# Performance work log

Hardware: AMD Instinct MI355X
Metric: run time of the kernel (lower is better)

Reference implementation:

```python
import jax, jax.numpy as jnp
import numpy as np

B, S, M, E, H = 4, 2048, 1024, 8, 4096
CAP = 2 * (B * S) // E  # GShard top-2 capacity = 2*s/e = 2048


def setup_inputs() -> dict:
    key = jax.random.key(0)
    k = jax.random.split(key, 6)
    sc = 0.02
    return {
        "x": jax.random.normal(k[0], (B, S, M), jnp.float32),
        "wg": jax.random.normal(k[1], (M, E), jnp.float32) * sc,
        "w1": jax.random.normal(k[2], (E, M, H), jnp.float32) * sc,
        "b1": jnp.zeros((E, H), jnp.float32),
        "w2": jax.random.normal(k[3], (E, H, M), jnp.float32) * sc,
        "b2": jnp.zeros((E, M), jnp.float32),
    }


def top2gating(logits, capacity):
    # Faithful GShard/fairscale top2gating: logits [s, e]
    s, e = logits.shape
    gates = jax.nn.softmax(logits, axis=-1)
    idx1 = jnp.argmax(gates, axis=1)
    mask1 = jax.nn.one_hot(idx1, e, dtype=jnp.float32)
    logits2 = jnp.where(mask1 > 0, -jnp.inf, logits)
    idx2 = jnp.argmax(logits2, axis=1)
    mask2 = jax.nn.one_hot(idx2, e, dtype=jnp.float32)
    # positions within each expert's buffer
    loc1 = jnp.cumsum(mask1, axis=0) - 1.0
    loc2 = jnp.cumsum(mask2, axis=0) - 1.0 + jnp.sum(mask1, axis=0, keepdims=True)
    # load-balancing aux loss (computed before capacity drop, per fairscale)
    me = jnp.mean(gates, axis=0)
    ce = jnp.mean(mask1, axis=0)
    l_aux = jnp.mean(me * ce) * (e * e)
    # drop tokens over capacity
    mask1 = mask1 * (loc1 < capacity)
    mask2 = mask2 * (loc2 < capacity)
    loc1_s = jnp.sum(loc1 * mask1, axis=1).astype(jnp.int32)
    loc2_s = jnp.sum(loc2 * mask2, axis=1).astype(jnp.int32)
    gates1 = jnp.sum(gates * mask1, axis=1)
    gates2 = jnp.sum(gates * mask2, axis=1)
    denom = jnp.maximum(gates1 + gates2, 1e-9)
    gates1 = gates1 / denom
    gates2 = gates2 / denom
    # dense [s, e, c] combine weights (as in the original einsum formulation)
    oh1 = jax.nn.one_hot(loc1_s, capacity, dtype=jnp.float32)
    oh2 = jax.nn.one_hot(loc2_s, capacity, dtype=jnp.float32)
    combine = (gates1[:, None] * mask1)[:, :, None] * oh1[:, None, :] \
            + (gates2[:, None] * mask2)[:, :, None] * oh2[:, None, :]
    dispatch = combine > 0
    return l_aux, combine, dispatch


def reference(x, wg, w1, b1, w2, b2):
    d_model = x.shape[2]
    xf = x.reshape(-1, d_model)                      # [s, m]
    logits = xf @ wg                                 # [s, e]
    l_aux, combine, dispatch = top2gating(logits, CAP)
    # dispatch: dense one-hot scatter, as in torch.einsum('sec,sm->ecm')
    disp = jnp.einsum('sec,sm->ecm', dispatch.astype(xf.dtype), xf)
    # per-expert FFN (Linear -> ReLU -> Linear), vectorized over experts
    h = jax.nn.relu(jnp.einsum('ecm,emh->ech', disp, w1) + b1[:, None, :])
    eo = jnp.einsum('ech,ehm->ecm', h, w2) + b2[:, None, :]
    # combine: torch.einsum('sec,ecm->sm')
    out = jnp.einsum('sec,ecm->sm', combine, eo)
    return out.reshape(x.shape), l_aux
```

## Files before the change

kernel.cpp:

```cpp
#include <hip/hip_runtime.h>
#include <stdint.h>

typedef unsigned short u16;
typedef __attribute__((ext_vector_type(8))) short bf16x8;
typedef __attribute__((ext_vector_type(4))) float f32x4;

#define TOKENS 8192
#define DM 1024
#define NE 8
#define DH 4096
#define CAP 2048

__device__ __forceinline__ u16 f2bf(float f) {
  unsigned int u = __float_as_uint(f);
  u = u + 0x7FFFu + ((u >> 16) & 1u);
  return (u16)(u >> 16);
}

__device__ __forceinline__ void gll16(const void* g, void* l) {
  __builtin_amdgcn_global_load_lds(
      (const __attribute__((address_space(1))) unsigned int*)g,
      (__attribute__((address_space(3))) unsigned int*)l, 16, 0, 0);
}

__global__ __launch_bounds__(256) void gating_kernel(
    const float* __restrict__ x, const float* __restrict__ wg,
    int* __restrict__ idx1, int* __restrict__ idx2,
    float* __restrict__ g1r, float* __restrict__ g2r, float* __restrict__ me) {
  __shared__ float gsh[4][8];
  int lane = threadIdx.x & 63;
  int w = threadIdx.x >> 6;
  int t = blockIdx.x * 4 + w;
  const float* xr = x + (size_t)t * DM;
  double acc[8];
#pragma unroll
  for (int e = 0; e < 8; ++e) acc[e] = 0.0;
#pragma unroll
  for (int it = 0; it < 4; ++it) {
    float4 xv = ((const float4*)xr)[it * 64 + lane];
    int base = (it * 64 + lane) * 4;
    const float* wr = wg + (size_t)base * 8;
    float xs[4] = {xv.x, xv.y, xv.z, xv.w};
#pragma unroll
    for (int j = 0; j < 4; ++j)
#pragma unroll
      for (int e = 0; e < 8; ++e) acc[e] += (double)xs[j] * (double)wr[j * 8 + e];
  }
#pragma unroll
  for (int off = 32; off > 0; off >>= 1)
#pragma unroll
    for (int e = 0; e < 8; ++e) acc[e] += __shfl_down(acc[e], off);
  if (lane == 0) {
    float l[8];
#pragma unroll
    for (int e = 0; e < 8; ++e) l[e] = (float)acc[e];
    int i1 = 0;
    float v1 = l[0];
#pragma unroll
    for (int e = 1; e < 8; ++e)
      if (l[e] > v1) { v1 = l[e]; i1 = e; }
    int i2 = -1;
    float v2 = -3.4e38f;
#pragma unroll
    for (int e = 0; e < 8; ++e)
      if (e != i1 && l[e] > v2) { v2 = l[e]; i2 = e; }
    float s = 0.f;
    float p[8];
#pragma unroll
    for (int e = 0; e < 8; ++e) { p[e] = expf(l[e] - v1); s += p[e]; }
    float inv = 1.f / s;
    idx1[t] = i1;
    idx2[t] = i2;
    g1r[t] = inv;
    g2r[t] = expf(v2 - v1) * inv;
#pragma unroll
    for (int e = 0; e < 8; ++e) gsh[w][e] = p[e] * inv;
  }
  __syncthreads();
  if (threadIdx.x < 8) {
    int e = threadIdx.x;
    atomicAdd(&me[e], gsh[0][e] + gsh[1][e] + gsh[2][e] + gsh[3][e]);
  }
}

__global__ __launch_bounds__(1024) void scan_kernel(
    const int* __restrict__ idx1, const int* __restrict__ idx2,
    const float* __restrict__ g1r, const float* __restrict__ g2r,
    const float* __restrict__ me,
    int* __restrict__ slot1, int* __restrict__ slot2,
    float* __restrict__ g1n, float* __restrict__ g2n,
    int* __restrict__ slot2tok, float* __restrict__ laux) {
  __shared__ u16 c[16][1024];
  __shared__ u16 csum[16][32];
  __shared__ int tot[16];
  int tid = threadIdx.x;
  int i1[8], i2[8];
#pragma unroll
  for (int ctr = 0; ctr < 16; ++ctr) c[ctr][tid] = 0;
#pragma unroll
  for (int j = 0; j < 8; ++j) {
    int t = tid * 8 + j;
    i1[j] = idx1[t];
    i2[j] = idx2[t];
    c[i1[j]][tid]++;
    c[8 + i2[j]][tid]++;
  }
  __syncthreads();
  if (tid < 512) {
    int ctr = tid >> 5, ch = tid & 31;
    int s = 0;
#pragma unroll
    for (int i = 0; i < 32; ++i) s += c[ctr][ch * 32 + i];
    csum[ctr][ch] = (u16)s;
  }
  __syncthreads();
  if (tid < 16) {
    int run = 0;
#pragma unroll
    for (int ch = 0; ch < 32; ++ch) {
      int v = csum[tid][ch];
      csum[tid][ch] = (u16)run;
      run += v;
    }
    tot[tid] = run;
  }
  __syncthreads();
  if (tid < 512) {
    int ctr = tid >> 5, ch = tid & 31;
    int run = csum[ctr][ch];
#pragma unroll
    for (int i = 0; i < 32; ++i) {
      int v = c[ctr][ch * 32 + i];
      c[ctr][ch * 32 + i] = (u16)run;
      run += v;
    }
  }
  __syncthreads();
#pragma unroll
  for (int j = 0; j < 8; ++j) {
    int t = tid * 8 + j;
    int e1 = i1[j], e2 = i2[j];
    int L1 = c[e1][tid]++;
    int L2 = c[8 + e2][tid]++;
    L2 += tot[e2];
    bool kv1 = L1 < CAP, kv2 = L2 < CAP;
    float G1 = kv1 ? g1r[t] : 0.f;
    float G2 = kv2 ? g2r[t] : 0.f;
    float den = fmaxf(G1 + G2, 1e-9f);
    g1n[t] = G1 / den;
    g2n[t] = G2 / den;
    int s1 = kv1 ? (e1 * CAP + L1) : -1;
    int s2 = kv2 ? (e2 * CAP + L2) : -1;
    slot1[t] = s1;
    slot2[t] = s2;
    if (kv1) slot2tok[s1] = t;
    if (kv2) slot2tok[s2] = t;
  }
  if (tid == 0) {
    double a = 0.0;
    for (int e = 0; e < 8; ++e)
      a += ((double)me[e] / 8192.0) * ((double)tot[e] / 8192.0);
    laux[0] = (float)(a * 8.0);
  }
}

__global__ void transpose_kernel(const float* __restrict__ src, u16* __restrict__ dst,
                                 int R, int C) {
  __shared__ float tile[32][33];
  int tx = threadIdx.x, ty = threadIdx.y;
  int r0 = blockIdx.y * 32, c0 = blockIdx.x * 32;
  const float* s = src + (size_t)blockIdx.z * R * C;
  u16* d = dst + (size_t)blockIdx.z * R * C;
#pragma unroll
  for (int i = 0; i < 32; i += 8) tile[ty + i][tx] = s[(size_t)(r0 + ty + i) * C + c0 + tx];
  __syncthreads();
#pragma unroll
  for (int i = 0; i < 32; i += 8)
    d[(size_t)(c0 + ty + i) * R + r0 + tx] = f2bf(tile[tx][ty + i]);
}

__global__ void gather_kernel(const float* __restrict__ x, const int* __restrict__ slot2tok,
                              u16* __restrict__ xe) {
  int slot = blockIdx.y * CAP + blockIdx.x;
  int tok = slot2tok[slot];
  int tid = threadIdx.x;
  u16 o[8];
  if (tok >= 0) {
    const float4* xr = (const float4*)(x + (size_t)tok * DM);
    float4 a = xr[tid * 2], b = xr[tid * 2 + 1];
    o[0] = f2bf(a.x); o[1] = f2bf(a.y); o[2] = f2bf(a.z); o[3] = f2bf(a.w);
    o[4] = f2bf(b.x); o[5] = f2bf(b.y); o[6] = f2bf(b.z); o[7] = f2bf(b.w);
  } else {
#pragma unroll
    for (int j = 0; j < 8; ++j) o[j] = 0;
  }
  *(uint4*)(xe + (size_t)slot * DM + tid * 8) = *(const uint4*)o;
}

#define BAR()                              \
  {                                        \
    asm volatile("" ::: "memory");         \
    __builtin_amdgcn_s_barrier();          \
    asm volatile("" ::: "memory");         \
  }
#define VMCNT(n) asm volatile("s_waitcnt vmcnt(" #n ")" ::: "memory")
#define LGKM(n) asm volatile("s_waitcnt lgkmcnt(" #n ")" ::: "memory")

template <int RELU, int OUTBF16>
__global__ __launch_bounds__(512, 2) void gemm_kernel(
    const u16* __restrict__ A, const u16* __restrict__ Bt,
    const float* __restrict__ bias, void* __restrict__ Cv,
    int MO, int NO, int K) {
  __shared__ __align__(16) u16 As[2][256 * 64];
  __shared__ __align__(16) u16 Bs[2][256 * 64];
  const int tid = threadIdx.x;
  const int lane = tid & 63, wid = tid >> 6;
  const int wm = wid >> 2, wn = wid & 3;

  const int gx = gridDim.x, gy = gridDim.y;
  const int nwg = gx * gy * gridDim.z;
  const int L = (blockIdx.z * gy + blockIdx.y) * gx + blockIdx.x;
  const int cpx = nwg >> 3;
  const int Ls = (L & 7) * cpx + (L >> 3);
  const int bx = Ls % gx;
  const int tq = Ls / gx;
  const int by = tq % gy;
  const int eb = tq / gy;

  const size_t Ks2 = (size_t)K * 2;
  const char* Ag = (const char*)(A + (size_t)eb * MO * K + (size_t)by * 256 * K);
  const char* Bg = (const char*)(Bt + (size_t)eb * NO * K + (size_t)bx * 256 * K);
  const int rl = tid >> 3;
  const int sb = ((tid & 7) * 16) ^ ((rl & 7) << 4);
  Ag += (size_t)rl * Ks2 + sb;
  Bg += (size_t)rl * Ks2 + sb;
  char* AsB = ((char*)As) + tid * 16;
  char* BsB = ((char*)Bs) + tid * 16;
  const u16* AsE = &As[0][0];
  const u16* BsE = &Bs[0][0];
  const int fr = lane & 15, kg8 = (lane >> 4) * 8;
  const int swz = (fr & 7) << 3;

#define STAGE_A(BUF_, REG_, KT_) \
  gll16(Ag + (size_t)((REG_)*64) * Ks2 + (size_t)(KT_)*128, AsB + (BUF_)*32768 + (REG_)*8192)
#define STAGE_B(BUF_, REG_, KT_) \
  gll16(Bg + (size_t)((REG_)*64) * Ks2 + (size_t)(KT_)*128, BsB + (BUF_)*32768 + (REG_)*8192)
#define LDA(BUF_, M_, K_) \
  (*(const bf16x8*)&AsE[(BUF_)*16384 + (wm * 128 + (M_)*16 + fr) * 64 + (((K_)*32 + kg8) ^ swz)])
#define LDB(BUF_, N_, K_) \
  (*(const bf16x8*)&BsE[(BUF_)*16384 + (wn * 64 + (N_)*16 + fr) * 64 + (((K_)*32 + kg8) ^ swz)])
#define MFMA_Q(MB_, NB_)                                                            \
  _Pragma("unroll") for (int k = 0; k < 2; ++k)                                     \
  _Pragma("unroll") for (int m = 0; m < 4; ++m)                                     \
  _Pragma("unroll") for (int n = 0; n < 2; ++n)                                     \
      acc[(MB_) + m][(NB_) + n] = __builtin_amdgcn_mfma_f32_16x16x32_bf16(          \
          areg[m][k], breg[(NB_) + n][k], acc[(MB_) + m][(NB_) + n], 0, 0, 0)

#define RD_A03(C_)                                                \
  _Pragma("unroll") for (int m = 0; m < 4; ++m) {                 \
    areg[m][0] = LDA(C_, m, 0); areg[m][1] = LDA(C_, m, 1);       \
  }
#define RD_A47(C_)                                                \
  _Pragma("unroll") for (int m = 0; m < 4; ++m) {                 \
    areg[m][0] = LDA(C_, 4 + m, 0); areg[m][1] = LDA(C_, 4 + m, 1); \
  }
#define RD_B01(C_)                                                \
  _Pragma("unroll") for (int n = 0; n < 2; ++n) {                 \
    breg[n][0] = LDB(C_, n, 0); breg[n][1] = LDB(C_, n, 1);       \
  }
#define RD_B23(C_)                                                \
  _Pragma("unroll") for (int n = 2; n < 4; ++n) {                 \
    breg[n][0] = LDB(C_, n, 0); breg[n][1] = LDB(C_, n, 1);       \
  }
#define MM(MB_, NB_)                          \
  BAR();                                      \
  LGKM(0);                                    \
  __builtin_amdgcn_sched_barrier(0);          \
  __builtin_amdgcn_s_setprio(1);              \
  MFMA_Q(MB_, NB_);                           \
  __builtin_amdgcn_s_setprio(0);              \
  BAR();

  f32x4 acc[8][4];
#pragma unroll
  for (int i = 0; i < 8; ++i)
#pragma unroll
    for (int j = 0; j < 4; ++j) acc[i][j] = {0.f, 0.f, 0.f, 0.f};
  bf16x8 areg[4][2], breg[4][2];

  const int NT = K >> 6;

  STAGE_A(0, 0, 0); STAGE_A(0, 1, 0); STAGE_A(0, 2, 0); STAGE_A(0, 3, 0);
  STAGE_B(0, 0, 0); STAGE_B(0, 1, 0); STAGE_B(0, 2, 0); STAGE_B(0, 3, 0);
  STAGE_A(1, 0, 1); STAGE_A(1, 2, 1);
  STAGE_B(1, 0, 1); STAGE_B(1, 1, 1);
  STAGE_B(1, 2, 1); STAGE_B(1, 3, 1);
  VMCNT(6);
  BAR();

  for (int t = 0; t < NT; t += 2) {
    const int t2 = (t + 2 < NT) ? t + 2 : NT - 2;
    const int t3 = (t + 3 < NT) ? t + 3 : NT - 1;
    RD_A03(0); RD_B01(0);
    STAGE_A(1, 1, t + 1); STAGE_A(1, 3, t + 1);
    LGKM(8);
    MM(0, 0);
    RD_B23(0);
    STAGE_A(0, 0, t2); STAGE_A(0, 2, t2);
    MM(0, 2);
    RD_A47(0);
    STAGE_B(0, 0, t2); STAGE_B(0, 1, t2);
    MM(4, 0);
    STAGE_B(0, 2, t2); STAGE_B(0, 3, t2);
    VMCNT(6);
    MM(4, 2);
    RD_A03(1); RD_B01(1);
    STAGE_A(0, 1, t2); STAGE_A(0, 3, t2);
    LGKM(8);
    MM(0, 0);
    RD_B23(1);
    STAGE_A(1, 0, t3); STAGE_A(1, 2, t3);
    MM(0, 2);
    RD_A47(1);
    STAGE_B(1, 0, t3); STAGE_B(1, 1, t3);
    MM(4, 0);
    STAGE_B(1, 2, t3); STAGE_B(1, 3, t3);
    VMCNT(6);
    MM(4, 2);
  }

  const int row0 = by * 256 + wm * 128 + (kg8 >> 3) * 4;
  const int col0 = bx * 256 + wn * 64 + fr;
  const float* be = bias + (size_t)eb * NO;
  size_t cbase = (size_t)eb * MO * NO;
#pragma unroll
  for (int m = 0; m < 8; ++m) {
#pragma unroll
    for (int n = 0; n < 4; ++n) {
      int col = col0 + n * 16;
      float bv = be[col];
#pragma unroll
      for (int r = 0; r < 4; ++r) {
        int row = row0 + m * 16 + r;
        float v = acc[m][n][r] + bv;
        if (RELU) v = fmaxf(v, 0.f);
        if (OUTBF16)
          ((u16*)Cv)[cbase + (size_t)row * NO + col] = f2bf(v);
        else
          ((float*)Cv)[cbase + (size_t)row * NO + col] = v;
      }
    }
  }
#undef MM
#undef RD_A03
#undef RD_A47
#undef RD_B01
#undef RD_B23
#undef STAGE_A
#undef STAGE_B
#undef LDA
#undef LDB
#undef MFMA_Q
}

__global__ void combine_kernel(const float* __restrict__ eo,
                               const float* __restrict__ g1n, const float* __restrict__ g2n,
                               const int* __restrict__ slot1, const int* __restrict__ slot2,
                               float* __restrict__ out) {
  int t = blockIdx.x, tid = threadIdx.x;
  float g1 = g1n[t], g2 = g2n[t];
  int s1 = slot1[t], s2 = slot2[t];
  float4 o = make_float4(0.f, 0.f, 0.f, 0.f);
  if (s1 >= 0) {
    float4 a = ((const float4*)(eo + (size_t)s1 * DM))[tid];
    o.x = g1 * a.x; o.y = g1 * a.y; o.z = g1 * a.z; o.w = g1 * a.w;
  }
  if (s2 >= 0) {
    float4 b = ((const float4*)(eo + (size_t)s2 * DM))[tid];
    o.x += g2 * b.x; o.y += g2 * b.y; o.z += g2 * b.z; o.w += g2 * b.w;
  }
  ((float4*)(out + (size_t)t * DM))[tid] = o;
}

extern "C" void kernel_launch(void* const* d_in, const int* in_sizes, int n_in,
                              void* d_out, int out_size, void* d_ws, size_t ws_size,
                              hipStream_t stream) {
  const float* x = (const float*)d_in[0];
  const float* wg = (const float*)d_in[1];
  const float* w1 = (const float*)d_in[2];
  const float* b1 = (const float*)d_in[3];
  const float* w2 = (const float*)d_in[4];
  const float* b2 = (const float*)d_in[5];
  float* out = (float*)d_out;

  const size_t SZ_WT1 = (size_t)NE * DH * DM * 2;
  const size_t SZ_WT2 = (size_t)NE * DM * DH * 2;
  const size_t SZ_XE = (size_t)NE * CAP * DM * 2;
  const size_t SZ_H = (size_t)NE * CAP * DH * 2;
  const size_t SZ_TOK = (size_t)TOKENS * 4;

  char* p = (char*)d_ws;
  u16* wt1 = (u16*)p;
  float* eo = (float*)p;            p += SZ_WT1;
  u16* wt2 = (u16*)p;               p += SZ_WT2;
  u16* xe = (u16*)p;                p += SZ_XE;
  u16* h = (u16*)p;                 p += SZ_H;
  int* idx1 = (int*)p;              p += SZ_TOK;
  int* idx2 = (int*)p;              p += SZ_TOK;
  int* slot1 = (int*)p;             p += SZ_TOK;
  int* slot2 = (int*)p;             p += SZ_TOK;
  float* g1r = (float*)p;           p += SZ_TOK;
  float* g2r = (float*)p;           p += SZ_TOK;
  float* g1n = (float*)p;           p += SZ_TOK;
  float* g2n = (float*)p;           p += SZ_TOK;
  int* slot2tok = (int*)p;          p += (size_t)NE * CAP * 4;
  float* me = (float*)p;            p += 256;
  if ((size_t)(p - (char*)d_ws) > ws_size) return;

  hipMemsetAsync(me, 0, 32, stream);
  hipMemsetAsync(slot2tok, 0xFF, (size_t)NE * CAP * 4, stream);

  gating_kernel<<<TOKENS / 4, 256, 0, stream>>>(x, wg, idx1, idx2, g1r, g2r, me);
  scan_kernel<<<1, 1024, 0, stream>>>(idx1, idx2, g1r, g2r, me, slot1, slot2, g1n, g2n,
                                      slot2tok, out + (size_t)TOKENS * DM);
  transpose_kernel<<<dim3(DH / 32, DM / 32, NE), dim3(32, 8), 0, stream>>>(w1, wt1, DM, DH);
  transpose_kernel<<<dim3(DM / 32, DH / 32, NE), dim3(32, 8), 0, stream>>>(w2, wt2, DH, DM);
  gather_kernel<<<dim3(CAP, NE), 128, 0, stream>>>(x, slot2tok, xe);
  gemm_kernel<1, 1><<<dim3(DH / 256, CAP / 256, NE), 512, 0, stream>>>(xe, wt1, b1, (void*)h,
                                                                       CAP, DH, DM);
  gemm_kernel<0, 0><<<dim3(DM / 256, CAP / 256, NE), 512, 0, stream>>>(h, wt2, b2, (void*)eo,
                                                                       CAP, DM, DH);
  combine_kernel<<<TOKENS, 256, 0, stream>>>(eo, g1n, g2n, slot1, slot2, out);
}
```

Baseline: 471.6 us.

## Fuse combine into second expert GEMM epilogue via gated atomic scatter-add

The second FFN GEMM now scatters its gate-weighted outputs straight into the token output rows with float atomicAdd, so the fp32 expert-output buffer and the separate combine kernel go away. The scan kernel writes one gate weight per expert slot instead of per-token slot and gate arrays, and the output is zeroed with a memset first. This saves a 64MB fp32 write plus re-read and one launch. In exchange the epilogue issues scattered 4-byte atomics, and the two-way sum order per token is no longer fixed.

```diff
diff --git a/kernel.cpp b/kernel.cpp
--- a/kernel.cpp
+++ b/kernel.cpp
@@ -87,9 +87,8 @@
     const int* __restrict__ idx1, const int* __restrict__ idx2,
     const float* __restrict__ g1r, const float* __restrict__ g2r,
     const float* __restrict__ me,
-    int* __restrict__ slot1, int* __restrict__ slot2,
-    float* __restrict__ g1n, float* __restrict__ g2n,
-    int* __restrict__ slot2tok, float* __restrict__ laux) {
+    int* __restrict__ slot2tok, float* __restrict__ gslot,
+    float* __restrict__ laux) {
   __shared__ u16 c[16][1024];
   __shared__ u16 csum[16][32];
   __shared__ int tot[16];
@@ -147,14 +146,16 @@
     float G1 = kv1 ? g1r[t] : 0.f;
     float G2 = kv2 ? g2r[t] : 0.f;
     float den = fmaxf(G1 + G2, 1e-9f);
-    g1n[t] = G1 / den;
-    g2n[t] = G2 / den;
-    int s1 = kv1 ? (e1 * CAP + L1) : -1;
-    int s2 = kv2 ? (e2 * CAP + L2) : -1;
-    slot1[t] = s1;
-    slot2[t] = s2;
-    if (kv1) slot2tok[s1] = t;
-    if (kv2) slot2tok[s2] = t;
+    if (kv1) {
+      int s1 = e1 * CAP + L1;
+      slot2tok[s1] = t;
+      gslot[s1] = G1 / den;
+    }
+    if (kv2) {
+      int s2 = e2 * CAP + L2;
+      slot2tok[s2] = t;
+      gslot[s2] = G2 / den;
+    }
   }
   if (tid == 0) {
     double a = 0.0;
@@ -206,11 +207,12 @@
 #define VMCNT(n) asm volatile("s_waitcnt vmcnt(" #n ")" ::: "memory")
 #define LGKM(n) asm volatile("s_waitcnt lgkmcnt(" #n ")" ::: "memory")
 
-template <int RELU, int OUTBF16>
+template <int RELU, int OUTMODE>
 __global__ __launch_bounds__(512, 2) void gemm_kernel(
     const u16* __restrict__ A, const u16* __restrict__ Bt,
     const float* __restrict__ bias, void* __restrict__ Cv,
-    int MO, int NO, int K) {
+    int MO, int NO, int K,
+    const int* __restrict__ s2t, const float* __restrict__ gsl) {
   __shared__ __align__(16) u16 As[2][256 * 64];
   __shared__ __align__(16) u16 Bs[2][256 * 64];
   const int tid = threadIdx.x;
@@ -332,22 +334,41 @@
   const int row0 = by * 256 + wm * 128 + (kg8 >> 3) * 4;
   const int col0 = bx * 256 + wn * 64 + fr;
   const float* be = bias + (size_t)eb * NO;
-  size_t cbase = (size_t)eb * MO * NO;
-#pragma unroll
-  for (int m = 0; m < 8; ++m) {
-#pragma unroll
-    for (int n = 0; n < 4; ++n) {
-      int col = col0 + n * 16;
-      float bv = be[col];
+  if (OUTMODE == 1) {
+    size_t cbase = (size_t)eb * MO * NO;
+#pragma unroll
+    for (int m = 0; m < 8; ++m) {
+#pragma unroll
+      for (int n = 0; n < 4; ++n) {
+        int col = col0 + n * 16;
+        float bv = be[col];
+#pragma unroll
+        for (int r = 0; r < 4; ++r) {
+          int row = row0 + m * 16 + r;
+          float v = acc[m][n][r] + bv;
+          if (RELU) v = fmaxf(v, 0.f);
+          ((u16*)Cv)[cbase + (size_t)row * NO + col] = f2bf(v);
+        }
+      }
+    }
+  } else {
+    float bv[4];
+#pragma unroll
+    for (int n = 0; n < 4; ++n) bv[n] = be[col0 + n * 16];
+#pragma unroll
+    for (int m = 0; m < 8; ++m) {
 #pragma unroll
       for (int r = 0; r < 4; ++r) {
-        int row = row0 + m * 16 + r;
-        float v = acc[m][n][r] + bv;
-        if (RELU) v = fmaxf(v, 0.f);
-        if (OUTBF16)
-          ((u16*)Cv)[cbase + (size_t)row * NO + col] = f2bf(v);
-        else
-          ((float*)Cv)[cbase + (size_t)row * NO + col] = v;
+        const int row = row0 + m * 16 + r;
+        const int slot = eb * CAP + row;
+        const int tok = s2t[slot];
+        if (tok >= 0) {
+          const float g = gsl[slot];
+          float* orow = ((float*)Cv) + (size_t)tok * DM;
+#pragma unroll
+          for (int n = 0; n < 4; ++n)
+            atomicAdd(orow + col0 + n * 16, g * (acc[m][n][r] + bv[n]));
+        }
       }
     }
   }
@@ -363,25 +384,6 @@
 #undef MFMA_Q
 }
 
-__global__ void combine_kernel(const float* __restrict__ eo,
-                               const float* __restrict__ g1n, const float* __restrict__ g2n,
-                               const int* __restrict__ slot1, const int* __restrict__ slot2,
-                               float* __restrict__ out) {
-  int t = blockIdx.x, tid = threadIdx.x;
-  float g1 = g1n[t], g2 = g2n[t];
-  int s1 = slot1[t], s2 = slot2[t];
-  float4 o = make_float4(0.f, 0.f, 0.f, 0.f);
-  if (s1 >= 0) {
-    float4 a = ((const float4*)(eo + (size_t)s1 * DM))[tid];
-    o.x = g1 * a.x; o.y = g1 * a.y; o.z = g1 * a.z; o.w = g1 * a.w;
-  }
-  if (s2 >= 0) {
-    float4 b = ((const float4*)(eo + (size_t)s2 * DM))[tid];
-    o.x += g2 * b.x; o.y += g2 * b.y; o.z += g2 * b.z; o.w += g2 * b.w;
-  }
-  ((float4*)(out + (size_t)t * DM))[tid] = o;
-}
-
 extern "C" void kernel_launch(void* const* d_in, const int* in_sizes, int n_in,
                               void* d_out, int out_size, void* d_ws, size_t ws_size,
                               hipStream_t stream) {
@@ -400,35 +402,31 @@
   const size_t SZ_TOK = (size_t)TOKENS * 4;
 
   char* p = (char*)d_ws;
-  u16* wt1 = (u16*)p;
-  float* eo = (float*)p;            p += SZ_WT1;
+  u16* wt1 = (u16*)p;               p += SZ_WT1;
   u16* wt2 = (u16*)p;               p += SZ_WT2;
   u16* xe = (u16*)p;                p += SZ_XE;
   u16* h = (u16*)p;                 p += SZ_H;
   int* idx1 = (int*)p;              p += SZ_TOK;
   int* idx2 = (int*)p;              p += SZ_TOK;
-  int* slot1 = (int*)p;             p += SZ_TOK;
-  int* slot2 = (int*)p;             p += SZ_TOK;
   float* g1r = (float*)p;           p += SZ_TOK;
   float* g2r = (float*)p;           p += SZ_TOK;
-  float* g1n = (float*)p;           p += SZ_TOK;
-  float* g2n = (float*)p;           p += SZ_TOK;
   int* slot2tok = (int*)p;          p += (size_t)NE * CAP * 4;
+  float* gslot = (float*)p;         p += (size_t)NE * CAP * 4;
   float* me = (float*)p;            p += 256;
   if ((size_t)(p - (char*)d_ws) > ws_size) return;
 
   hipMemsetAsync(me, 0, 32, stream);
   hipMemsetAsync(slot2tok, 0xFF, (size_t)NE * CAP * 4, stream);
+  hipMemsetAsync(out, 0, (size_t)TOKENS * DM * 4, stream);
 
   gating_kernel<<<TOKENS / 4, 256, 0, stream>>>(x, wg, idx1, idx2, g1r, g2r, me);
-  scan_kernel<<<1, 1024, 0, stream>>>(idx1, idx2, g1r, g2r, me, slot1, slot2, g1n, g2n,
-                                      slot2tok, out + (size_t)TOKENS * DM);
+  scan_kernel<<<1, 1024, 0, stream>>>(idx1, idx2, g1r, g2r, me, slot2tok, gslot,
+                                      out + (size_t)TOKENS * DM);
   transpose_kernel<<<dim3(DH / 32, DM / 32, NE), dim3(32, 8), 0, stream>>>(w1, wt1, DM, DH);
   transpose_kernel<<<dim3(DM / 32, DH / 32, NE), dim3(32, 8), 0, stream>>>(w2, wt2, DH, DM);
   gather_kernel<<<dim3(CAP, NE), 128, 0, stream>>>(x, slot2tok, xe);
-  gemm_kernel<1, 1><<<dim3(DH / 256, CAP / 256, NE), 512, 0, stream>>>(xe, wt1, b1, (void*)h,
-                                                                       CAP, DH, DM);
-  gemm_kernel<0, 0><<<dim3(DM / 256, CAP / 256, NE), 512, 0, stream>>>(h, wt2, b2, (void*)eo,
-                                                                       CAP, DM, DH);
-  combine_kernel<<<TOKENS, 256, 0, stream>>>(eo, g1n, g2n, slot1, slot2, out);
-}
+  gemm_kernel<1, 1><<<dim3(DH / 256, CAP / 256, NE), 512, 0, stream>>>(
+      xe, wt1, b1, (void*)h, CAP, DH, DM, nullptr, nullptr);
+  gemm_kernel<0, 2><<<dim3(DM / 256, CAP / 256, NE), 512, 0, stream>>>(
+      h, wt2, b2, (void*)out, CAP, DM, DH, slot2tok, gslot);
+}
```

Result: slower. 499.7 us (+6.0%).
